# Performance work log

Measured on AMD Instinct MI355X. Metric: run time of the kernel, lower is better.

## Reference

```python
import jax, jax.numpy as jnp
import numpy as np


def conv1x1(x, w, b):
    # x: (B,C,H,W), w: (Cout,Cin), b: (Cout,) -- 1x1 conv == channel matmul
    return jnp.einsum('bchw,oc->bohw', x, w) + b[None, :, None, None]


def spatial_gate(q_feat, k_feat, scale):
    # Faithful to: matmul over flattened (B*HW, C) x (C, B*HW), then
    # max over keys, mean over the batch axis, softmax over spatial dims.
    B, C, H, W = q_feat.shape
    q = q_feat.reshape(B, C, H * W).transpose(0, 2, 1).reshape(B * H * W, C)
    k = k_feat.reshape(B, C, H * W).transpose(1, 0, 2).reshape(C, B * H * W)
    s = (q @ k).reshape(B * H * W, B, H * W)          # (BHW, B, HW)
    m = jnp.mean(jnp.max(s, axis=-1), axis=-1)        # (BHW,)
    w = jax.nn.softmax(m.reshape(B, H * W) * scale, axis=-1)
    return w.reshape(B, 1, H, W)


def setup_inputs() -> dict:
    key = jax.random.key(0)
    ks = jax.random.split(key, 10)
    C = 256
    shp = (8, C, 32, 32)
    inp = {
        'x4': jax.random.normal(ks[0], shp, jnp.float32),
        'x3': jax.random.normal(ks[1], shp, jnp.float32),
        'wq': jax.random.normal(ks[2], (C, C), jnp.float32) * 0.02,
        'bq': jnp.zeros((C,), jnp.float32),
        'wk': jax.random.normal(ks[3], (C, C), jnp.float32) * 0.02,
        'bk': jnp.zeros((C,), jnp.float32),
        'wv': jax.random.normal(ks[4], (C, C), jnp.float32) * 0.02,
        'bv': jnp.zeros((C,), jnp.float32),
        'w128': jax.random.normal(ks[5], (128, C), jnp.float32) * 0.02,
        'b128': jnp.zeros((128,), jnp.float32),
    }
    return inp


def reference(x4, x3, wq, bq, wk, bk, wv, bv, w128, b128):
    C = x4.shape[1]
    scale = 1.0 / (C ** 0.5)
    # shared QKV 1x1 convs applied to both inputs
    aq = conv1x1(x4, wq, bq)
    ak = conv1x1(x4, wk, bk)
    av = conv1x1(x4, wv, bv)
    bq_f = conv1x1(x3, wq, bq)
    bk_f = conv1x1(x3, wk, bk)
    bv_f = conv1x1(x3, wv, bv)
    # four gating branches: self-self (a), self-self (b), cross a->b, cross b->a
    a_x4 = conv1x1(spatial_gate(aq, ak, scale) * av, w128, b128)
    b_x3 = conv1x1(spatial_gate(bq_f, bk_f, scale) * bv_f, w128, b128)
    x43 = conv1x1(spatial_gate(aq, bk_f, scale) * bv_f, w128, b128)
    x34 = conv1x1(spatial_gate(bq_f, ak, scale) * av, w128, b128)
    # cat order: [x34, a_x4] then [x43, b_x3]
    ab_cat = jnp.concatenate([x34, a_x4, x43, b_x3], axis=1)  # (B,512,H,W)
    # Block2D loop: block class undefined in source; surrogate = identity
    # (ab12 = concat of the two chunks == ab_cat), applied depth=4 times.
    ab12 = ab_cat
    ab12 = ab_cat * ab12
    ab_avg = jnp.mean(ab12, axis=(2, 3), keepdims=True)        # (B,512,1,1)
    ab = jax.nn.softmax(ab_avg, axis=-1)   # softmax over size-1 axis -> ones
    final = ab * ab_cat
    return final
```

## Files before the change

kernel.cpp:

```cpp
#include <hip/hip_runtime.h>

typedef unsigned short ushort_t;
typedef unsigned char uchar_t;
typedef __attribute__((ext_vector_type(8))) short bf16x8;
typedef __attribute__((ext_vector_type(4))) float f32x4;
typedef __attribute__((ext_vector_type(16))) float f32x16;
typedef __attribute__((ext_vector_type(8))) int v8i;

__device__ __forceinline__ unsigned short f2bf(float f) {
  union { float f; unsigned int u; } v; v.f = f;
  unsigned int r = v.u + 0x7FFFu + ((v.u >> 16) & 1u);
  return (unsigned short)(r >> 16);
}

__device__ __forceinline__ float bf2f(unsigned short u) {
  union { unsigned int i; float f; } v; v.i = ((unsigned int)u) << 16;
  return v.f;
}

__device__ __forceinline__ void gl_lds16(const void* gsrc, void* ldst) {
  __builtin_amdgcn_global_load_lds(
      (const __attribute__((address_space(1))) void*)gsrc,
      (__attribute__((address_space(3))) void*)ldst, 16, 0, 0);
}

__device__ __forceinline__ int frag_idx(int oc, int ci) {
  return (((oc>>4)*8 + (ci>>5))<<9) + ((((ci>>3)&3)*16 + (oc&15))<<3) + (ci&7);
}

__global__ __launch_bounds__(256) void k1_weights(
    const float* __restrict__ wq, const float* __restrict__ bq,
    const float* __restrict__ wk, const float* __restrict__ bk,
    const float* __restrict__ wv, const float* __restrict__ bv,
    const float* __restrict__ w128,
    ushort_t* __restrict__ Wf, float* __restrict__ bias_all)
{
  const int ci = threadIdx.x;
  if (blockIdx.x < 512) {
    const int oc = blockIdx.x;
    const float v = (oc < 256) ? wq[oc*256 + ci] : wk[(oc-256)*256 + ci];
    Wf[frag_idx(oc, ci)] = f2bf(v);
    if (ci == 0) bias_all[oc] = (oc < 256) ? bq[oc] : bk[oc-256];
  } else {
    const int og = (blockIdx.x - 512) * 4;
    float a0 = 0.f, a1 = 0.f, a2 = 0.f, a3 = 0.f;
    for (int co = 0; co < 256; co++) {
      const float wvv = wv[co*256 + ci];
      a0 += w128[(og+0)*256 + co] * wvv;
      a1 += w128[(og+1)*256 + co] * wvv;
      a2 += w128[(og+2)*256 + co] * wvv;
      a3 += w128[(og+3)*256 + co] * wvv;
    }
    Wf[frag_idx(512+og+0, ci)] = f2bf(a0);
    Wf[frag_idx(512+og+1, ci)] = f2bf(a1);
    Wf[frag_idx(512+og+2, ci)] = f2bf(a2);
    Wf[frag_idx(512+og+3, ci)] = f2bf(a3);
    if (ci < 4) {
      float s = 0.f;
      for (int co = 0; co < 256; co++) s += w128[(og+ci)*256 + co] * bv[co];
      bias_all[512 + og + ci] = s;
    }
  }
}

__global__ __launch_bounds__(256) void k2_features(
    const float* __restrict__ x4, const float* __restrict__ x3,
    const ushort_t* __restrict__ Wf, const float* __restrict__ bias_all,
    uchar_t* __restrict__ Qf8, uchar_t* __restrict__ Kf8, float* __restrict__ V)
{
  __shared__ ushort_t Af[32*512];
  __shared__ ushort_t Wl[2][32*512];
  __shared__ ushort_t Lt[64*72];

  const int tid = threadIdx.x;
  const int w = tid >> 6, lane = tid & 63;
  const int mrow = lane & 15, quad = lane >> 4;
  const int ln31 = lane & 31, half = lane >> 5;

  const int px0 = blockIdx.x * 64;
  const int src = px0 >> 13, b = (px0 >> 10) & 7, hw0 = px0 & 1023;
  const float* xp = (src ? x3 : x4) + (size_t)b*262144;

  const int ot0 = blockIdx.y * 5;

  for (int kb = 0; kb < 8; kb++)
    gl_lds16(Wf + ((size_t)((ot0*4 + w)*8 + kb)<<9) + lane*8,
             &Wl[ot0&1][(w*8+kb)*512]);

  {
    const int hw = hw0 + w*16 + mrow;
    for (int kb = 0; kb < 8; kb++) {
      const int ch0 = kb*32 + quad*8;
      bf16x8 pk;
      #pragma unroll
      for (int j = 0; j < 8; j++)
        ((ushort_t*)&pk)[j] = f2bf(xp[(size_t)(ch0 + j)*1024 + hw]);
      *(bf16x8*)&Af[(w*8 + kb)*512 + lane*8] = pk;
    }
  }
  __syncthreads();

  for (int ot = ot0; ot < ot0 + 5; ot++) {
    const int nbuf = (ot+1) & 1, cbuf = ot & 1;
    if (ot + 1 < ot0 + 5) {
      for (int kb = 0; kb < 8; kb++)
        gl_lds16(Wf + ((size_t)(((ot+1)*4 + w)*8 + kb)<<9) + lane*8,
                 &Wl[nbuf][(w*8+kb)*512]);
      asm volatile("s_waitcnt vmcnt(8)" ::: "memory");
    } else {
      asm volatile("s_waitcnt vmcnt(0)" ::: "memory");
    }

    f32x4 acc[4];
    #pragma unroll
    for (int lg = 0; lg < 4; lg++) acc[lg] = (f32x4){0.f,0.f,0.f,0.f};
    #pragma unroll
    for (int kb = 0; kb < 8; kb++) {
      const bf16x8 a = *(const bf16x8*)&Wl[cbuf][(w*8 + kb)*512 + lane*8];
      #pragma unroll
      for (int lg = 0; lg < 4; lg++) {
        const bf16x8 bx = *(const bf16x8*)&Af[(lg*8 + kb)*512 + lane*8];
        acc[lg] = __builtin_amdgcn_mfma_f32_16x16x32_bf16(a, bx, acc[lg], 0, 0, 0);
      }
    }
    const int ocl = w*16 + quad*4;
    const float4 bias4 = *(const float4*)&bias_all[ot*64 + ocl];

    if (ot < 8) {
      __syncthreads();
      #pragma unroll
      for (int lg = 0; lg < 4; lg++) {
        const int px = lg*16 + mrow;
        ushort4 pk;
        pk.x = f2bf(acc[lg][0] + bias4.x);
        pk.y = f2bf(acc[lg][1] + bias4.y);
        pk.z = f2bf(acc[lg][2] + bias4.z);
        pk.w = f2bf(acc[lg][3] + bias4.w);
        *(ushort4*)&Lt[px*72 + ocl] = pk;
      }
      __syncthreads();
      const int g = w >> 1, e = w & 1;
      const int row = g*32 + ln31;
      const ushort_t* lp = &Lt[row*72 + e*32 + half*8];
      float fl[8], fh[8];
      #pragma unroll
      for (int j = 0; j < 8; j++) { fl[j] = bf2f(lp[j]); fh[j] = bf2f(lp[16+j]); }
      int w0 = __builtin_amdgcn_cvt_pk_fp8_f32(fl[0], fl[1], 0, 0);
      w0     = __builtin_amdgcn_cvt_pk_fp8_f32(fl[2], fl[3], w0, 1);
      int w1 = __builtin_amdgcn_cvt_pk_fp8_f32(fl[4], fl[5], 0, 0);
      w1     = __builtin_amdgcn_cvt_pk_fp8_f32(fl[6], fl[7], w1, 1);
      int w2 = __builtin_amdgcn_cvt_pk_fp8_f32(fh[0], fh[1], 0, 0);
      w2     = __builtin_amdgcn_cvt_pk_fp8_f32(fh[2], fh[3], w2, 1);
      int w3 = __builtin_amdgcn_cvt_pk_fp8_f32(fh[4], fh[5], 0, 0);
      w3     = __builtin_amdgcn_cvt_pk_fp8_f32(fh[6], fh[7], w3, 1);
      uchar_t* dst = (ot < 4) ? Qf8 : Kf8;
      const size_t chunk = (size_t)((px0>>5) + g)*8 + (ot&3)*2 + e;
      int4 pk4; pk4.x = w0; pk4.y = w1; pk4.z = w2; pk4.w = w3;
      *(int4*)(dst + (chunk<<10) + lane*16) = pk4;
    } else {
      const int ocv0 = (ot-8)*64 + ocl;
      float* vb = V + (((size_t)(src*8 + b)*128) << 10) + hw0;
      #pragma unroll
      for (int lg = 0; lg < 4; lg++) {
        vb[(size_t)(ocv0+0)*1024 + lg*16 + mrow] = acc[lg][0] + bias4.x;
        vb[(size_t)(ocv0+1)*1024 + lg*16 + mrow] = acc[lg][1] + bias4.y;
        vb[(size_t)(ocv0+2)*1024 + lg*16 + mrow] = acc[lg][2] + bias4.z;
        vb[(size_t)(ocv0+3)*1024 + lg*16 + mrow] = acc[lg][3] + bias4.w;
      }
    }
  }
}

__global__ __launch_bounds__(256, 2) void k3_smax(
    const uchar_t* __restrict__ Qf8, const uchar_t* __restrict__ Kf8,
    float* __restrict__ Pm)
{
  __shared__ __align__(16) uchar_t Kl[2][32768];

  const int tid = threadIdx.x;
  const int bt = blockIdx.x >> 6;
  const int rt = blockIdx.x & 63;
  const int w = tid >> 6, lane = tid & 63;
  const int ln31 = lane & 31, half = lane >> 5;

  const int rgb = rt*8 + w*2;
  const int ph = (blockIdx.x & 1)*4;

  #pragma unroll
  for (int q = 0; q < 8; q++) {
    const int c = w*8 + q;
    const int cg = bt*32 + ph*4 + (c>>3);
    gl_lds16(Kf8 + (((size_t)cg*8 + (c&7))<<10) + lane*16, &Kl[0][c*1024]);
  }

  v8i qa[2][4];
  #pragma unroll
  for (int rg = 0; rg < 2; rg++)
    #pragma unroll
    for (int u = 0; u < 4; u++) {
      const int4 p0 = *(const int4*)(Qf8 + (((size_t)(rgb + rg)*8 + 2*u+0)<<10) + lane*16);
      const int4 p1 = *(const int4*)(Qf8 + (((size_t)(rgb + rg)*8 + 2*u+1)<<10) + lane*16);
      qa[rg][u] = (v8i){p0.x, p0.y, p0.z, p0.w, p1.x, p1.y, p1.z, p1.w};
    }

  f32x16 zv;
  #pragma unroll
  for (int i = 0; i < 16; i++) zv[i] = 0.f;
  f32x16 rmax0, rmax1;
  #pragma unroll
  for (int i = 0; i < 16; i++) { rmax0[i] = -3.4e38f; rmax1[i] = -3.4e38f; }

  for (int s = 0; s < 8; s++) {
    __syncthreads();
    if (s < 7) {
      const int sn = (s + 1 + ph) & 7;
      #pragma unroll
      for (int q = 0; q < 8; q++) {
        const int c = w*8 + q;
        const int cg = bt*32 + sn*4 + (c>>3);
        gl_lds16(Kf8 + (((size_t)cg*8 + (c&7))<<10) + lane*16,
                 &Kl[(s+1)&1][c*1024]);
      }
    }
    const uchar_t* kl = Kl[s & 1];
    #pragma unroll
    for (int cgl = 0; cgl < 4; cgl++) {
      f32x16 a0 = zv, a1 = zv;
      #pragma unroll
      for (int u = 0; u < 4; u++) {
        const int4 b0 = *(const int4*)&kl[(cgl*8 + 2*u+0)*1024 + lane*16];
        const int4 b1 = *(const int4*)&kl[(cgl*8 + 2*u+1)*1024 + lane*16];
        const v8i bu = (v8i){b0.x, b0.y, b0.z, b0.w, b1.x, b1.y, b1.z, b1.w};
        a0 = __builtin_amdgcn_mfma_scale_f32_32x32x64_f8f6f4(
            qa[0][u], bu, a0, 0, 0, 0, 0x7F7F7F7F, 0, 0x7F7F7F7F);
        a1 = __builtin_amdgcn_mfma_scale_f32_32x32x64_f8f6f4(
            qa[1][u], bu, a1, 0, 0, 0, 0x7F7F7F7F, 0, 0x7F7F7F7F);
      }
      #pragma unroll
      for (int i = 0; i < 16; i++) {
        rmax0[i] = fmaxf(rmax0[i], a0[i]);
        rmax1[i] = fmaxf(rmax1[i], a1[i]);
      }
    }
  }

  #pragma unroll
  for (int rg = 0; rg < 2; rg++) {
    #pragma unroll
    for (int e = 0; e < 16; e++) {
      float v = (rg == 0) ? rmax0[e] : rmax1[e];
      v = fmaxf(v, __shfl_xor(v, 1));
      v = fmaxf(v, __shfl_xor(v, 2));
      v = fmaxf(v, __shfl_xor(v, 4));
      v = fmaxf(v, __shfl_xor(v, 8));
      v = fmaxf(v, __shfl_xor(v, 16));
      if (ln31 == 0) {
        const int row = rt*256 + w*64 + rg*32 + (e&3) + 8*(e>>2) + 4*half;
        Pm[(size_t)bt*16384 + row] = v;
      }
    }
  }
}

__global__ __launch_bounds__(1024) void k4_gates(
    const float* __restrict__ Pm, float* __restrict__ G)
{
  __shared__ float red[1024];
  const int tid = threadIdx.x;
  const int qset = blockIdx.x >> 3, b = blockIdx.x & 7;
  const int i = qset*8192 + b*1024 + tid;

  float ma = 0.f, mb = 0.f;
  #pragma unroll
  for (int bt = 0; bt < 8; bt++)  ma += Pm[(size_t)bt*16384 + i];
  #pragma unroll
  for (int bt = 8; bt < 16; bt++) mb += Pm[(size_t)bt*16384 + i];
  const float sc = 0.125f * 0.0625f;
  const float la = ma * sc, lb = mb * sc;

  red[tid] = la; __syncthreads();
  for (int s = 512; s > 0; s >>= 1) { if (tid < s) red[tid] = fmaxf(red[tid], red[tid+s]); __syncthreads(); }
  const float Ma = red[0]; __syncthreads();
  const float ea = expf(la - Ma);
  red[tid] = ea; __syncthreads();
  for (int s = 512; s > 0; s >>= 1) { if (tid < s) red[tid] += red[tid+s]; __syncthreads(); }
  const float ga = ea / red[0]; __syncthreads();

  red[tid] = lb; __syncthreads();
  for (int s = 512; s > 0; s >>= 1) { if (tid < s) red[tid] = fmaxf(red[tid], red[tid+s]); __syncthreads(); }
  const float Mb = red[0]; __syncthreads();
  const float eb = expf(lb - Mb);
  red[tid] = eb; __syncthreads();
  for (int s = 512; s > 0; s >>= 1) { if (tid < s) red[tid] += red[tid+s]; __syncthreads(); }
  const float gb = eb / red[0];

  G[(size_t)(qset*2 + 0)*8192 + b*1024 + tid] = ga;
  G[(size_t)(qset*2 + 1)*8192 + b*1024 + tid] = gb;
}

__global__ __launch_bounds__(256) void k5_out(
    const float* __restrict__ V, const float* __restrict__ G,
    const float* __restrict__ b128, float* __restrict__ out)
{
  const int idx = blockIdx.x*256 + threadIdx.x;
  const int flat = idx << 2;
  const int hw = flat & 1023;
  const int ch = (flat >> 10) & 511;
  const int b  = flat >> 19;
  const int blk = ch >> 7, o = ch & 127;
  const int gidx = (blk == 0) ? 2 : (blk == 1) ? 0 : (blk == 2) ? 1 : 3;
  const int src = (blk >= 2) ? 1 : 0;

  const float4 v = *(const float4*)&V[((size_t)((src*8 + b)*128 + o) << 10) + hw];
  const float4 g = *(const float4*)&G[(size_t)gidx*8192 + b*1024 + hw];
  const float bias = b128[o];
  float4 r;
  r.x = g.x*v.x + bias; r.y = g.y*v.y + bias;
  r.z = g.z*v.z + bias; r.w = g.w*v.w + bias;
  *(float4*)&out[flat] = r;
}

extern "C" void kernel_launch(void* const* d_in, const int* in_sizes, int n_in,
                              void* d_out, int out_size, void* d_ws, size_t ws_size,
                              hipStream_t stream)
{
  const float* x4   = (const float*)d_in[0];
  const float* x3   = (const float*)d_in[1];
  const float* wq   = (const float*)d_in[2];
  const float* bq   = (const float*)d_in[3];
  const float* wk   = (const float*)d_in[4];
  const float* bk   = (const float*)d_in[5];
  const float* wv   = (const float*)d_in[6];
  const float* bv   = (const float*)d_in[7];
  const float* w128 = (const float*)d_in[8];
  const float* b128 = (const float*)d_in[9];
  float* out = (float*)d_out;

  char* ws = (char*)d_ws;
  uchar_t*  Qf8 = (uchar_t*)ws;  ws += (size_t)512*8*1024;
  uchar_t*  Kf8 = (uchar_t*)ws;  ws += (size_t)512*8*1024;
  float*    V   = (float*)ws;    ws += (size_t)2*8*128*1024*4;
  float*    Pm  = (float*)ws;    ws += (size_t)16*16384*4;
  ushort_t* Wf  = (ushort_t*)ws; ws += (size_t)640*256*2;
  float* bias_all = (float*)ws;  ws += 640*4;
  float*    G   = (float*)ws;

  k1_weights <<<544,          256, 0, stream>>>(wq, bq, wk, bk, wv, bv, w128, Wf, bias_all);
  k2_features<<<dim3(256, 2), 256, 0, stream>>>(x4, x3, Wf, bias_all, Qf8, Kf8, V);
  k3_smax    <<<1024,         256, 0, stream>>>(Qf8, Kf8, Pm);
  k4_gates   <<<16,          1024, 0, stream>>>(Pm, G);
  k5_out     <<<4096,         256, 0, stream>>>(V, G, b128, out);
}
```

Measured before the change: 204.7 us.

## Fuse gate softmax into output kernel and spread weight folding across blocks

Removes the separate 16-block gate-softmax kernel. Each output block now recomputes the mean of maxima and the softmax for its 1024-pixel gate row using wave shuffles, then applies it to V directly, so the G buffer and one launch go away. The folded w128·wv weight computation now uses one block per output row (640 blocks instead of 544), which gives more parallelism. The k3 occupancy hint drops from 2 to 1, which frees registers but may lower residency. The cost is redundant softmax work: every channel block rereads 8×4 KB of Pm.

```diff
diff --git a/kernel.cpp b/kernel.cpp
--- a/kernel.cpp
+++ b/kernel.cpp
@@ -36,29 +36,21 @@
     ushort_t* __restrict__ Wf, float* __restrict__ bias_all)
 {
   const int ci = threadIdx.x;
-  if (blockIdx.x < 512) {
-    const int oc = blockIdx.x;
+  const int oc = blockIdx.x;
+  if (oc < 512) {
     const float v = (oc < 256) ? wq[oc*256 + ci] : wk[(oc-256)*256 + ci];
     Wf[frag_idx(oc, ci)] = f2bf(v);
     if (ci == 0) bias_all[oc] = (oc < 256) ? bq[oc] : bk[oc-256];
   } else {
-    const int og = (blockIdx.x - 512) * 4;
-    float a0 = 0.f, a1 = 0.f, a2 = 0.f, a3 = 0.f;
-    for (int co = 0; co < 256; co++) {
-      const float wvv = wv[co*256 + ci];
-      a0 += w128[(og+0)*256 + co] * wvv;
-      a1 += w128[(og+1)*256 + co] * wvv;
-      a2 += w128[(og+2)*256 + co] * wvv;
-      a3 += w128[(og+3)*256 + co] * wvv;
-    }
-    Wf[frag_idx(512+og+0, ci)] = f2bf(a0);
-    Wf[frag_idx(512+og+1, ci)] = f2bf(a1);
-    Wf[frag_idx(512+og+2, ci)] = f2bf(a2);
-    Wf[frag_idx(512+og+3, ci)] = f2bf(a3);
-    if (ci < 4) {
+    const int o = oc - 512;
+    const float* wr = w128 + (size_t)o*256;
+    float a = 0.f;
+    for (int co = 0; co < 256; co++) a += wr[co] * wv[co*256 + ci];
+    Wf[frag_idx(oc, ci)] = f2bf(a);
+    if (ci == 0) {
       float s = 0.f;
-      for (int co = 0; co < 256; co++) s += w128[(og+ci)*256 + co] * bv[co];
-      bias_all[512 + og + ci] = s;
+      for (int co = 0; co < 256; co++) s += wr[co] * bv[co];
+      bias_all[oc] = s;
     }
   }
 }
@@ -171,7 +163,7 @@
   }
 }
 
-__global__ __launch_bounds__(256, 2) void k3_smax(
+__global__ __launch_bounds__(256, 1) void k3_smax(
     const uchar_t* __restrict__ Qf8, const uchar_t* __restrict__ Kf8,
     float* __restrict__ Pm)
 {
@@ -262,62 +254,54 @@
   }
 }
 
-__global__ __launch_bounds__(1024) void k4_gates(
-    const float* __restrict__ Pm, float* __restrict__ G)
-{
-  __shared__ float red[1024];
+__global__ __launch_bounds__(256) void k5_out(
+    const float* __restrict__ V, const float* __restrict__ Pm,
+    const float* __restrict__ b128, float* __restrict__ out)
+{
+  __shared__ float xw[2][4];
   const int tid = threadIdx.x;
-  const int qset = blockIdx.x >> 3, b = blockIdx.x & 7;
-  const int i = qset*8192 + b*1024 + tid;
-
-  float ma = 0.f, mb = 0.f;
-  #pragma unroll
-  for (int bt = 0; bt < 8; bt++)  ma += Pm[(size_t)bt*16384 + i];
-  #pragma unroll
-  for (int bt = 8; bt < 16; bt++) mb += Pm[(size_t)bt*16384 + i];
-  const float sc = 0.125f * 0.0625f;
-  const float la = ma * sc, lb = mb * sc;
-
-  red[tid] = la; __syncthreads();
-  for (int s = 512; s > 0; s >>= 1) { if (tid < s) red[tid] = fmaxf(red[tid], red[tid+s]); __syncthreads(); }
-  const float Ma = red[0]; __syncthreads();
-  const float ea = expf(la - Ma);
-  red[tid] = ea; __syncthreads();
-  for (int s = 512; s > 0; s >>= 1) { if (tid < s) red[tid] += red[tid+s]; __syncthreads(); }
-  const float ga = ea / red[0]; __syncthreads();
-
-  red[tid] = lb; __syncthreads();
-  for (int s = 512; s > 0; s >>= 1) { if (tid < s) red[tid] = fmaxf(red[tid], red[tid+s]); __syncthreads(); }
-  const float Mb = red[0]; __syncthreads();
-  const float eb = expf(lb - Mb);
-  red[tid] = eb; __syncthreads();
-  for (int s = 512; s > 0; s >>= 1) { if (tid < s) red[tid] += red[tid+s]; __syncthreads(); }
-  const float gb = eb / red[0];
-
-  G[(size_t)(qset*2 + 0)*8192 + b*1024 + tid] = ga;
-  G[(size_t)(qset*2 + 1)*8192 + b*1024 + tid] = gb;
-}
-
-__global__ __launch_bounds__(256) void k5_out(
-    const float* __restrict__ V, const float* __restrict__ G,
-    const float* __restrict__ b128, float* __restrict__ out)
-{
-  const int idx = blockIdx.x*256 + threadIdx.x;
-  const int flat = idx << 2;
-  const int hw = flat & 1023;
-  const int ch = (flat >> 10) & 511;
-  const int b  = flat >> 19;
+  const int ch = blockIdx.x & 511, b = blockIdx.x >> 9;
   const int blk = ch >> 7, o = ch & 127;
   const int gidx = (blk == 0) ? 2 : (blk == 1) ? 0 : (blk == 2) ? 1 : 3;
   const int src = (blk >= 2) ? 1 : 0;
-
-  const float4 v = *(const float4*)&V[((size_t)((src*8 + b)*128 + o) << 10) + hw];
-  const float4 g = *(const float4*)&G[(size_t)gidx*8192 + b*1024 + hw];
+  const int qset = gidx >> 1, side = gidx & 1;
+
+  const float4* Pm4 = (const float4*)(Pm + (size_t)side*8*16384 + qset*8192 + b*1024);
+  float4 l = {0.f, 0.f, 0.f, 0.f};
+  #pragma unroll
+  for (int t = 0; t < 8; t++) {
+    const float4 p = Pm4[t*4096 + tid];
+    l.x += p.x; l.y += p.y; l.z += p.z; l.w += p.w;
+  }
+  const float sc = 0.125f * 0.0625f;
+  l.x *= sc; l.y *= sc; l.z *= sc; l.w *= sc;
+
+  const int w = tid >> 6, lane = tid & 63;
+  float m = fmaxf(fmaxf(l.x, l.y), fmaxf(l.z, l.w));
+  #pragma unroll
+  for (int d = 1; d < 64; d <<= 1) m = fmaxf(m, __shfl_xor(m, d));
+  if (lane == 0) xw[0][w] = m;
+  __syncthreads();
+  m = fmaxf(fmaxf(xw[0][0], xw[0][1]), fmaxf(xw[0][2], xw[0][3]));
+
+  float4 e;
+  e.x = expf(l.x - m); e.y = expf(l.y - m);
+  e.z = expf(l.z - m); e.w = expf(l.w - m);
+  float s = e.x + e.y + e.z + e.w;
+  #pragma unroll
+  for (int d = 1; d < 64; d <<= 1) s += __shfl_xor(s, d);
+  if (lane == 0) xw[1][w] = s;
+  __syncthreads();
+  s = xw[1][0] + xw[1][1] + xw[1][2] + xw[1][3];
+  const float inv = 1.f / s;
+
+  const int hw0 = tid << 2;
+  const float4 v = *(const float4*)&V[((size_t)((src*8 + b)*128 + o) << 10) + hw0];
   const float bias = b128[o];
   float4 r;
-  r.x = g.x*v.x + bias; r.y = g.y*v.y + bias;
-  r.z = g.z*v.z + bias; r.w = g.w*v.w + bias;
-  *(float4*)&out[flat] = r;
+  r.x = e.x*inv*v.x + bias; r.y = e.y*inv*v.y + bias;
+  r.z = e.z*inv*v.z + bias; r.w = e.w*inv*v.w + bias;
+  *(float4*)&out[((size_t)(b*512 + ch) << 10) + hw0] = r;
 }
 
 extern "C" void kernel_launch(void* const* d_in, const int* in_sizes, int n_in,
@@ -342,12 +326,10 @@
   float*    V   = (float*)ws;    ws += (size_t)2*8*128*1024*4;
   float*    Pm  = (float*)ws;    ws += (size_t)16*16384*4;
   ushort_t* Wf  = (ushort_t*)ws; ws += (size_t)640*256*2;
-  float* bias_all = (float*)ws;  ws += 640*4;
-  float*    G   = (float*)ws;
-
-  k1_weights <<<544,          256, 0, stream>>>(wq, bq, wk, bk, wv, bv, w128, Wf, bias_all);
+  float* bias_all = (float*)ws;
+
+  k1_weights <<<640,          256, 0, stream>>>(wq, bq, wk, bk, wv, bv, w128, Wf, bias_all);
   k2_features<<<dim3(256, 2), 256, 0, stream>>>(x4, x3, Wf, bias_all, Qf8, Kf8, V);
   k3_smax    <<<1024,         256, 0, stream>>>(Qf8, Kf8, Pm);
-  k4_gates   <<<16,          1024, 0, stream>>>(Pm, G);
-  k5_out     <<<4096,         256, 0, stream>>>(V, G, b128, out);
-}
+  k5_out     <<<4096,         256, 0, stream>>>(V, Pm, b128, out);
+}
```

Measured after the change: 208.7 us. Within noise of the previous version (+2.0%).
